# Performance work log

Measured on AMD Instinct MI355X. Metric: run time of the kernel, lower is better.

The kernel has to match this reference:

```python
import jax, jax.numpy as jnp
import numpy as np

B, A, NC, DIR, LMAX, MAXZ, NORB = 8, 64, 128, 4, 2, 10, 14
NF = NC * DIR * (2 * LMAX + 1)   # 2560
O2 = NORB * NORB                 # 196
AO = A * NORB                    # 896
LOG2 = float(np.log(2.0))

def ssp(v):  # spk shifted softplus
    return jax.nn.softplus(v) - LOG2

def setup_inputs():
    key = jax.random.key(0)
    ks = jax.random.split(key, 12)
    Z = jax.random.randint(ks[0], (B, A), 1, MAXZ)
    idx = np.arange(A)
    nbh_np = np.stack([np.delete(idx, i) for i in range(A)], 0)  # [A, A-1]: all atoms except self
    nbh = jnp.asarray(np.broadcast_to(nbh_np[None], (B, A, A - 1)).copy(), dtype=jnp.int32)
    x = jax.random.normal(ks[1], (B, A, NC), jnp.float32)
    Vijkl = jax.random.normal(ks[2], (B, A, A - 1, NF), jnp.float32) * 0.1
    sc = 1.0 / np.sqrt(NF)
    W_off = jax.random.normal(ks[3], (NF, O2), jnp.float32) * sc
    b_off = jnp.zeros((O2,), jnp.float32)
    W_on = jax.random.normal(ks[4], (NF, O2), jnp.float32) * sc
    b_on = jnp.zeros((O2,), jnp.float32)
    W_ovoff = jax.random.normal(ks[5], (NF, O2), jnp.float32) * sc
    b_ovoff = jnp.zeros((O2,), jnp.float32)
    ov_emb = jax.random.normal(ks[6], (MAXZ, O2), jnp.float32) * 0.1  # trainable overlap onsite embedding
    orb_energies = jax.random.normal(ks[7], (MAXZ, NORB), jnp.float32)  # h0 energies
    s0_energies = jnp.ones((MAXZ, NORB), jnp.float32)                   # s0 init = ones
    W1 = jax.random.normal(ks[8], (NC, NC // 2), jnp.float32) / np.sqrt(NC)
    b1 = jnp.zeros((NC // 2,), jnp.float32)
    W2 = jax.random.normal(ks[9], (NC // 2, 1), jnp.float32) / np.sqrt(NC // 2)
    b2 = jnp.zeros((1,), jnp.float32)
    return {"Z": Z, "nbh": nbh, "x": x, "Vijkl": Vijkl,
            "W_off": W_off, "b_off": b_off, "W_on": W_on, "b_on": b_on,
            "W_ovoff": W_ovoff, "b_ovoff": b_ovoff, "ov_emb": ov_emb,
            "orb_energies": orb_energies, "s0_energies": s0_energies,
            "W1": W1, "b1": b1, "W2": W2, "b2": b2}

def reference(Z, nbh, x, Vijkl, W_off, b_off, W_on, b_on, W_ovoff, b_ovoff,
              ov_emb, orb_energies, s0_energies, W1, b1, W2, b2):
    # permutation that reorders neighbor slots (plus appended zero/self slot) into atom order
    ar = jnp.broadcast_to(jnp.arange(A, dtype=nbh.dtype)[None, :, None], (B, A, 1))
    sort_idx = jnp.argsort(jnp.concatenate([nbh, ar], axis=2), axis=2)  # [B,A,A]
    eyeA = jnp.eye(A, dtype=Vijkl.dtype)
    eyeAO = jnp.eye(AO, dtype=Vijkl.dtype)

    def assemble(off, on):
        # off: [B,A,A-1,O2] pair blocks; on: [B,A,O2] onsite blocks
        offz = jnp.concatenate([off, jnp.zeros((B, A, 1, O2), off.dtype)], axis=2)  # zero self block at slot A-1
        offg = jnp.take_along_axis(offz, sort_idx[..., None], axis=2)               # [B,A,A,O2]
        M = offg + eyeA[None, :, :, None] * on[:, :, None, :]
        M = M.reshape(B, A, A, NORB, NORB).transpose(0, 1, 3, 2, 4).reshape(B, AO, AO)
        return 0.5 * (M + M.transpose(0, 2, 1))

    # Hamiltonian: offsite Dense + onsite Dense mean-aggregated over pairs
    H_off = Vijkl @ W_off + b_off                       # [B,A,A-1,O2]
    H_on = jnp.mean(Vijkl @ W_on + b_on, axis=2)        # [B,A,O2]
    H = assemble(H_off, H_on)
    # h0 single-atom diagonal (orb mask is all-active -> full diagonal)
    H = H + eyeAO[None] * orb_energies[Z].reshape(B, 1, AO)

    # Overlap: offsite Dense + onsite embedding lookup
    S_off = Vijkl @ W_ovoff + b_ovoff
    S_on = ov_emb[Z]                                    # [B,A,O2]
    S = assemble(S_off, S_on)
    S = S + eyeAO[None] * s0_energies[Z].reshape(B, 1, AO)

    # energy head: Dense->ssp->Dense->ScaleShift(0,1), sum over atoms
    Ei = ssp(x @ W1 + b1) @ W2 + b2                     # [B,A,1]
    E = jnp.sum(Ei, axis=1)                             # [B,1]
    return H, S, E
```

## Files before the change

### kernel.cpp

```cpp
#include <hip/hip_runtime.h>

#define B_      8
#define A_      64
#define NPAIR   63
#define NC_     128
#define NF_     2560
#define O2_     196
#define NORB_   14
#define AO_     896
#define NCOLS   588
#define CSTRIDE 640
#define KSTEPS  80
#define BM      128
#define BN      640
#define BSTEP_BYTES 40960

typedef short bf16x8 __attribute__((ext_vector_type(8)));
typedef float f32x4  __attribute__((ext_vector_type(4)));

__device__ __forceinline__ unsigned f2bf(float f) {
    unsigned u = __builtin_bit_cast(unsigned, f);
    return (u + 0x7fffu + ((u >> 16) & 1u)) >> 16;
}

__global__ void prep_w(const float* __restrict__ W_off, const float* __restrict__ W_ovoff,
                       const float* __restrict__ W_on, unsigned short* __restrict__ Bws) {
    __shared__ float wt[32 * BN];
    const int ks = blockIdx.x, t = threadIdx.x;
    for (int e = t; e < 32 * BN; e += 256) {
        int kl = e / BN, c = e - kl * BN;
        int kg = ks * 32 + kl;
        float v = 0.f;
        if (c < O2_)          v = W_off  [(size_t)kg * O2_ + c];
        else if (c < 2 * O2_) v = W_ovoff[(size_t)kg * O2_ + (c - O2_)];
        else if (c < 3 * O2_) v = W_on   [(size_t)kg * O2_ + (c - 2 * O2_)];
        wt[kl * BN + c] = v;
    }
    __syncthreads();
    unsigned short* out = Bws + (size_t)ks * (BN * 32);
    for (int e = t; e < BN * 4; e += 256) {
        int n = e >> 2, sg = e & 3;
        uint4 w;
        w.x = f2bf(wt[(sg * 8 + 0) * BN + n]) | (f2bf(wt[(sg * 8 + 1) * BN + n]) << 16);
        w.y = f2bf(wt[(sg * 8 + 2) * BN + n]) | (f2bf(wt[(sg * 8 + 3) * BN + n]) << 16);
        w.z = f2bf(wt[(sg * 8 + 4) * BN + n]) | (f2bf(wt[(sg * 8 + 5) * BN + n]) << 16);
        w.w = f2bf(wt[(sg * 8 + 6) * BN + n]) | (f2bf(wt[(sg * 8 + 7) * BN + n]) << 16);
        *(uint4*)(out + (size_t)n * 32 + sg * 8) = w;
    }
}

__global__ __launch_bounds__(512, 2)
void gemm_off(const float* __restrict__ V, const unsigned short* __restrict__ Bws,
              const float* __restrict__ b_off, const float* __restrict__ b_ovoff,
              const float* __restrict__ b_on, float* __restrict__ HSoff) {
    __shared__ alignas(16) unsigned short Alds[2][BM * 32];

    const int tid  = threadIdx.x;
    const int mt   = blockIdx.x;
    const int lane = tid & 63;
    const int wv   = tid >> 6;
    const int wm   = wv >> 2, wn = wv & 3;

    const int arow = tid >> 2, aseg = tid & 3;
    const float* aptr = V + (size_t)(mt * BM + arow) * NF_ + aseg * 8;

    const char* bp = (const char*)Bws + (size_t)(wn * 160 + (lane & 15)) * 64 + (lane >> 4) * 16;
#define BFRAG(t_, nf_) (*(const bf16x8*)(bp + (size_t)(t_) * BSTEP_BYTES + (nf_) * 1024))

    f32x4 acc[4][10];
#pragma unroll
    for (int mf = 0; mf < 4; ++mf)
#pragma unroll
        for (int nf = 0; nf < 10; ++nf)
            acc[mf][nf] = (f32x4){0.f, 0.f, 0.f, 0.f};

    float4 pv0, pv1;
    auto loadA = [&](int ks) {
        const float* s = aptr + ks * 32;
        pv0 = ((const float4*)s)[0];
        pv1 = ((const float4*)s)[1];
    };
    auto writeA = [&](int bf) {
        uint4 w;
        w.x = f2bf(pv0.x) | (f2bf(pv0.y) << 16);
        w.y = f2bf(pv0.z) | (f2bf(pv0.w) << 16);
        w.z = f2bf(pv1.x) | (f2bf(pv1.y) << 16);
        w.w = f2bf(pv1.z) | (f2bf(pv1.w) << 16);
        unsigned byte = ((unsigned)(arow * 64 + aseg * 16)) ^ ((unsigned)(arow & 7) << 4);
        *(uint4*)((char*)&Alds[bf][0] + byte) = w;
    };

    const int ar = wm * 64 + (lane & 15);
    const unsigned kb = (unsigned)(lane >> 4) * 16;

#define ARD(mf_) (*(const bf16x8*)((const char*)Ab + ((((unsigned)((ar + (mf_) * 16) * 64) + kb)) ^ ((unsigned)(ar & 7) << 4))))

#define MFMA4(bv_, nf_) {                                                                  \
    acc[0][nf_] = __builtin_amdgcn_mfma_f32_16x16x32_bf16(af0, bv_, acc[0][nf_], 0, 0, 0); \
    acc[1][nf_] = __builtin_amdgcn_mfma_f32_16x16x32_bf16(af1, bv_, acc[1][nf_], 0, 0, 0); \
    acc[2][nf_] = __builtin_amdgcn_mfma_f32_16x16x32_bf16(af2, bv_, acc[2][nf_], 0, 0, 0); \
    acc[3][nf_] = __builtin_amdgcn_mfma_f32_16x16x32_bf16(af3, bv_, acc[3][nf_], 0, 0, 0); }

    bf16x8 bq0, bq1, bq2, bq3, bq4;

    loadA(0);
    writeA(0);
    bq0 = BFRAG(0, 0); bq1 = BFRAG(0, 1); bq2 = BFRAG(0, 2); bq3 = BFRAG(0, 3); bq4 = BFRAG(0, 4);
    loadA(1);
    asm volatile("s_waitcnt lgkmcnt(0)" ::: "memory");
    __builtin_amdgcn_s_barrier();
    __builtin_amdgcn_sched_barrier(0);

    int cur = 0;
    for (int t = 0; t < KSTEPS; ++t) {
        const unsigned short* Ab = &Alds[cur][0];
        bf16x8 af0 = ARD(0), af1 = ARD(1), af2 = ARD(2), af3 = ARD(3);

        MFMA4(bq0, 0); bq0 = BFRAG(t, 5);
        MFMA4(bq1, 1); bq1 = BFRAG(t, 6);
        MFMA4(bq2, 2); bq2 = BFRAG(t, 7);
        MFMA4(bq3, 3); bq3 = BFRAG(t, 8);
        MFMA4(bq4, 4); bq4 = BFRAG(t, 9);
        MFMA4(bq0, 5); bq0 = BFRAG(t + 1, 0);
        MFMA4(bq1, 6); bq1 = BFRAG(t + 1, 1);
        MFMA4(bq2, 7); bq2 = BFRAG(t + 1, 2);
        MFMA4(bq3, 8); bq3 = BFRAG(t + 1, 3);
        MFMA4(bq4, 9); bq4 = BFRAG(t + 1, 4);

        if (t < KSTEPS - 1) {
            writeA(cur ^ 1);
            int ks2 = t + 2 < KSTEPS ? t + 2 : KSTEPS - 1;
            loadA(ks2);
            asm volatile("s_waitcnt lgkmcnt(0)" ::: "memory");
            __builtin_amdgcn_s_barrier();
            __builtin_amdgcn_sched_barrier(0);
        }
        cur ^= 1;
    }

    const int c16 = lane & 15, rg = lane >> 4;
#pragma unroll
    for (int nf = 0; nf < 10; ++nf) {
        int C = wn * 160 + nf * 16 + c16;
        if (C >= NCOLS) continue;
        float bias = (C < O2_) ? b_off[C] : (C < 2 * O2_) ? b_ovoff[C - O2_] : b_on[C - 2 * O2_];
#pragma unroll
        for (int mf = 0; mf < 4; ++mf) {
            int R = mt * BM + wm * 64 + mf * 16 + rg * 4;
            float* o = HSoff + (size_t)R * CSTRIDE + C;
            o[0]           = acc[mf][nf][0] + bias;
            o[CSTRIDE]     = acc[mf][nf][1] + bias;
            o[2 * CSTRIDE] = acc[mf][nf][2] + bias;
            o[3 * CSTRIDE] = acc[mf][nf][3] + bias;
        }
    }
#undef BFRAG
#undef ARD
#undef MFMA4
}

__global__ void hon_reduce(const float* __restrict__ HSoff, float* __restrict__ Hon) {
    const int g = blockIdx.x;
    const int t = threadIdx.x;
    if (t >= O2_) return;
    const float* p0 = HSoff + (size_t)g * NPAIR * CSTRIDE + 2 * O2_ + t;
    const float* p1 = p0 + (size_t)21 * CSTRIDE;
    const float* p2 = p0 + (size_t)42 * CSTRIDE;
    float a0 = 0.f, a1 = 0.f, a2 = 0.f;
#pragma unroll 3
    for (int j = 0; j < 21; ++j) {
        a0 += p0[0]; a1 += p1[0]; a2 += p2[0];
        p0 += CSTRIDE; p1 += CSTRIDE; p2 += CSTRIDE;
    }
    Hon[(size_t)g * O2_ + t] = (a0 + a1 + a2) * (1.f / (float)NPAIR);
}

__global__ __launch_bounds__(256)
void assemble_k(const float* __restrict__ HSoff, const float* __restrict__ Hon,
                const int* __restrict__ Z, const float* __restrict__ ov_emb,
                const float* __restrict__ orbE, const float* __restrict__ s0E,
                float* __restrict__ H, float* __restrict__ S) {
    __shared__ float Ai[NPAIR * 197];
    __shared__ float Bj[2][16 * 200];
    __shared__ float Dg[O2_];
    __shared__ float Dd[NORB_];

    const int bid = blockIdx.x;
    const int h = bid & 1, i = (bid >> 1) & 63, b = bid >> 7;
    const int t = threadIdx.x;
    const int g = b * A_ + i;
    const int z = Z[g];
    float* out = (h ? S : H) + (size_t)b * AO_ * AO_;

    const float* abase = HSoff + (size_t)g * NPAIR * CSTRIDE + h * O2_;
    for (int u = t; u < NPAIR * O2_; u += 256) {
        int jj = u / O2_, e = u - jj * O2_;
        Ai[jj * 197 + e] = abase[(size_t)jj * CSTRIDE + e];
    }
    if (t < O2_)   Dg[t] = h ? ov_emb[(size_t)z * O2_ + t]   : Hon[(size_t)g * O2_ + t];
    if (t < NORB_) Dd[t] = h ? s0E[(size_t)z * NORB_ + t]    : orbE[(size_t)z * NORB_ + t];

    auto stageB = [&](int buf, int jc) {
        for (int u = t; u < 16 * O2_; u += 256) {
            int jl = u / O2_, e = u - jl * O2_;
            int j = jc * 16 + jl;
            if (j != i) {
                int idx = (i < j) ? i : i - 1;
                Bj[buf][jl * 200 + e] =
                    HSoff[((size_t)(b * A_ + j) * NPAIR + idx) * CSTRIDE + h * O2_ + e];
            }
        }
    };
    stageB(0, 0);
    __syncthreads();

    const int tj = t / NORB_, tq = t - tj * NORB_;
    for (int jc = 0; jc < 4; ++jc) {
        if (jc < 3) stageB((jc + 1) & 1, jc + 1);
        if (t < 224) {
            const int j = jc * 16 + tj;
            const int cur = jc & 1;
#pragma unroll
            for (int p = 0; p < NORB_; ++p) {
                float v;
                if (j == i) {
                    v = 0.5f * (Dg[p * NORB_ + tq] + Dg[tq * NORB_ + p]);
                    if (p == tq) v += Dd[p];
                } else {
                    int jj = (j < i) ? j : j - 1;
                    v = 0.5f * (Ai[jj * 197 + p * NORB_ + tq] + Bj[cur][tj * 200 + tq * NORB_ + p]);
                }
                out[(size_t)(i * NORB_ + p) * AO_ + jc * 224 + t] = v;
            }
        }
        __syncthreads();
    }
}

__global__ void energy_k(const float* __restrict__ x, const float* __restrict__ W1,
                         const float* __restrict__ b1, const float* __restrict__ W2,
                         const float* __restrict__ b2, float* __restrict__ E) {
    __shared__ float partial[8];
    const int b = blockIdx.x;
    const int lane = threadIdx.x & 63;
    const int w = threadIdx.x >> 6;
    float esum = 0.f;
    for (int aa = 0; aa < 8; ++aa) {
        const int a = w * 8 + aa;
        const float* xr = x + (size_t)(b * A_ + a) * NC_;
        float hj = b1[lane];
        for (int k = 0; k < NC_; ++k) hj = fmaf(xr[k], W1[k * 64 + lane], hj);
        float sp = fmaxf(hj, 0.f) + log1pf(expf(-fabsf(hj))) - 0.69314718055994531f;
        float v = sp * W2[lane];
        for (int off = 32; off; off >>= 1) v += __shfl_down(v, off);
        if (lane == 0) esum += v + b2[0];
    }
    if (lane == 0) partial[w] = esum;
    __syncthreads();
    if (threadIdx.x == 0) {
        float e = 0.f;
        for (int k = 0; k < 8; ++k) e += partial[k];
        E[b] = e;
    }
}

extern "C" void kernel_launch(void* const* d_in, const int* in_sizes, int n_in,
                              void* d_out, int out_size, void* d_ws, size_t ws_size,
                              hipStream_t stream) {
    const int*   Z       = (const int*)  d_in[0];
    const float* x       = (const float*)d_in[2];
    const float* V       = (const float*)d_in[3];
    const float* W_off   = (const float*)d_in[4];
    const float* b_off   = (const float*)d_in[5];
    const float* W_on    = (const float*)d_in[6];
    const float* b_on    = (const float*)d_in[7];
    const float* W_ovoff = (const float*)d_in[8];
    const float* b_ovoff = (const float*)d_in[9];
    const float* ov_emb  = (const float*)d_in[10];
    const float* orbE    = (const float*)d_in[11];
    const float* s0E     = (const float*)d_in[12];
    const float* W1      = (const float*)d_in[13];
    const float* b1      = (const float*)d_in[14];
    const float* W2      = (const float*)d_in[15];
    const float* b2      = (const float*)d_in[16];

    float* H = (float*)d_out;
    float* S = H + (size_t)B_ * AO_ * AO_;
    float* E = S + (size_t)B_ * AO_ * AO_;

    char* ws = (char*)d_ws;
    unsigned short* Bws = (unsigned short*)ws;
    float* HSoff = (float*)(ws + (size_t)4  * 1024 * 1024);
    float* Hon   = (float*)(ws + (size_t)88 * 1024 * 1024);

    prep_w    <<<KSTEPS, 256, 0, stream>>>(W_off, W_ovoff, W_on, Bws);
    gemm_off  <<<252,    512, 0, stream>>>(V, Bws, b_off, b_ovoff, b_on, HSoff);
    hon_reduce<<<512,    256, 0, stream>>>(HSoff, Hon);
    assemble_k<<<1024,   256, 0, stream>>>(HSoff, Hon, Z, ov_emb, orbE, s0E, H, S);
    energy_k  <<<8,      512, 0, stream>>>(x, W1, b1, W2, b2, E);
}
```

Measured before the change: 307.5 us.

## Halve GEMM M-tile to 64 rows and fuse energy head into weight-prep kernel

The GEMM row tile drops from 128 to 64, so the grid doubles to 504 blocks and each wave holds half as many accumulators. Launch bounds rise to 4 blocks per SM, and the A-tile staging and swizzle indexing are reworked to match. The aim is to fill more of the CUs, since 252 blocks leave many idle, at the cost of reloading each B fragment for fewer rows. The energy head is merged into the weight-prep kernel as extra blocks to save one launch.

Measured after the change: 361.5 us. 17.6% more time.

```diff
diff --git a/kernel.cpp b/kernel.cpp
--- a/kernel.cpp
+++ b/kernel.cpp
@@ -11,7 +11,7 @@
 #define NCOLS   588
 #define CSTRIDE 640
 #define KSTEPS  80
-#define BM      128
+#define BM      64
 #define BN      640
 #define BSTEP_BYTES 40960
 
@@ -23,33 +23,63 @@
     return (u + 0x7fffu + ((u >> 16) & 1u)) >> 16;
 }
 
-__global__ void prep_w(const float* __restrict__ W_off, const float* __restrict__ W_ovoff,
-                       const float* __restrict__ W_on, unsigned short* __restrict__ Bws) {
-    __shared__ float wt[32 * BN];
-    const int ks = blockIdx.x, t = threadIdx.x;
-    for (int e = t; e < 32 * BN; e += 256) {
-        int kl = e / BN, c = e - kl * BN;
-        int kg = ks * 32 + kl;
-        float v = 0.f;
-        if (c < O2_)          v = W_off  [(size_t)kg * O2_ + c];
-        else if (c < 2 * O2_) v = W_ovoff[(size_t)kg * O2_ + (c - O2_)];
-        else if (c < 3 * O2_) v = W_on   [(size_t)kg * O2_ + (c - 2 * O2_)];
-        wt[kl * BN + c] = v;
-    }
-    __syncthreads();
-    unsigned short* out = Bws + (size_t)ks * (BN * 32);
-    for (int e = t; e < BN * 4; e += 256) {
-        int n = e >> 2, sg = e & 3;
-        uint4 w;
-        w.x = f2bf(wt[(sg * 8 + 0) * BN + n]) | (f2bf(wt[(sg * 8 + 1) * BN + n]) << 16);
-        w.y = f2bf(wt[(sg * 8 + 2) * BN + n]) | (f2bf(wt[(sg * 8 + 3) * BN + n]) << 16);
-        w.z = f2bf(wt[(sg * 8 + 4) * BN + n]) | (f2bf(wt[(sg * 8 + 5) * BN + n]) << 16);
-        w.w = f2bf(wt[(sg * 8 + 6) * BN + n]) | (f2bf(wt[(sg * 8 + 7) * BN + n]) << 16);
-        *(uint4*)(out + (size_t)n * 32 + sg * 8) = w;
-    }
-}
-
-__global__ __launch_bounds__(512, 2)
+__global__ __launch_bounds__(512)
+void prep_energy(const float* __restrict__ W_off, const float* __restrict__ W_ovoff,
+                 const float* __restrict__ W_on, unsigned short* __restrict__ Bws,
+                 const float* __restrict__ x, const float* __restrict__ W1,
+                 const float* __restrict__ b1, const float* __restrict__ W2,
+                 const float* __restrict__ b2, float* __restrict__ E) {
+    const int t = threadIdx.x;
+    if (blockIdx.x < KSTEPS) {
+        __shared__ float wt[32 * BN];
+        const int ks = blockIdx.x;
+        for (int e = t; e < 32 * BN; e += 512) {
+            int kl = e / BN, c = e - kl * BN;
+            int kg = ks * 32 + kl;
+            float v = 0.f;
+            if (c < O2_)          v = W_off  [(size_t)kg * O2_ + c];
+            else if (c < 2 * O2_) v = W_ovoff[(size_t)kg * O2_ + (c - O2_)];
+            else if (c < 3 * O2_) v = W_on   [(size_t)kg * O2_ + (c - 2 * O2_)];
+            wt[kl * BN + c] = v;
+        }
+        __syncthreads();
+        unsigned short* out = Bws + (size_t)ks * (BN * 32);
+        for (int e = t; e < BN * 4; e += 512) {
+            int n = e >> 2, sg = e & 3;
+            uint4 w;
+            w.x = f2bf(wt[(sg * 8 + 0) * BN + n]) | (f2bf(wt[(sg * 8 + 1) * BN + n]) << 16);
+            w.y = f2bf(wt[(sg * 8 + 2) * BN + n]) | (f2bf(wt[(sg * 8 + 3) * BN + n]) << 16);
+            w.z = f2bf(wt[(sg * 8 + 4) * BN + n]) | (f2bf(wt[(sg * 8 + 5) * BN + n]) << 16);
+            w.w = f2bf(wt[(sg * 8 + 6) * BN + n]) | (f2bf(wt[(sg * 8 + 7) * BN + n]) << 16);
+            *(uint4*)(out + (size_t)n * 32 + sg * 8) = w;
+        }
+    } else {
+        __shared__ float partial[8];
+        const int b = blockIdx.x - KSTEPS;
+        const int lane = t & 63;
+        const int w = t >> 6;
+        float esum = 0.f;
+        for (int aa = 0; aa < 8; ++aa) {
+            const int a = w * 8 + aa;
+            const float* xr = x + (size_t)(b * A_ + a) * NC_;
+            float hj = b1[lane];
+            for (int k = 0; k < NC_; ++k) hj = fmaf(xr[k], W1[k * 64 + lane], hj);
+            float sp = fmaxf(hj, 0.f) + log1pf(expf(-fabsf(hj))) - 0.69314718055994531f;
+            float v = sp * W2[lane];
+            for (int off = 32; off; off >>= 1) v += __shfl_down(v, off);
+            if (lane == 0) esum += v + b2[0];
+        }
+        if (lane == 0) partial[w] = esum;
+        __syncthreads();
+        if (t == 0) {
+            float e = 0.f;
+            for (int k = 0; k < 8; ++k) e += partial[k];
+            E[b] = e;
+        }
+    }
+}
+
+__global__ __launch_bounds__(512, 4)
 void gemm_off(const float* __restrict__ V, const unsigned short* __restrict__ Bws,
               const float* __restrict__ b_off, const float* __restrict__ b_ovoff,
               const float* __restrict__ b_on, float* __restrict__ HSoff) {
@@ -61,45 +91,39 @@
     const int wv   = tid >> 6;
     const int wm   = wv >> 2, wn = wv & 3;
 
-    const int arow = tid >> 2, aseg = tid & 3;
-    const float* aptr = V + (size_t)(mt * BM + arow) * NF_ + aseg * 8;
+    const int arow = tid >> 3, aseg = tid & 7;
+    const float* aptr = V + (size_t)(mt * BM + arow) * NF_ + aseg * 4;
 
     const char* bp = (const char*)Bws + (size_t)(wn * 160 + (lane & 15)) * 64 + (lane >> 4) * 16;
 #define BFRAG(t_, nf_) (*(const bf16x8*)(bp + (size_t)(t_) * BSTEP_BYTES + (nf_) * 1024))
 
-    f32x4 acc[4][10];
-#pragma unroll
-    for (int mf = 0; mf < 4; ++mf)
+    f32x4 acc[2][10];
+#pragma unroll
+    for (int mf = 0; mf < 2; ++mf)
 #pragma unroll
         for (int nf = 0; nf < 10; ++nf)
             acc[mf][nf] = (f32x4){0.f, 0.f, 0.f, 0.f};
 
-    float4 pv0, pv1;
+    float4 pv;
     auto loadA = [&](int ks) {
-        const float* s = aptr + ks * 32;
-        pv0 = ((const float4*)s)[0];
-        pv1 = ((const float4*)s)[1];
+        pv = *(const float4*)(aptr + ks * 32);
     };
     auto writeA = [&](int bf) {
-        uint4 w;
-        w.x = f2bf(pv0.x) | (f2bf(pv0.y) << 16);
-        w.y = f2bf(pv0.z) | (f2bf(pv0.w) << 16);
-        w.z = f2bf(pv1.x) | (f2bf(pv1.y) << 16);
-        w.w = f2bf(pv1.z) | (f2bf(pv1.w) << 16);
-        unsigned byte = ((unsigned)(arow * 64 + aseg * 16)) ^ ((unsigned)(arow & 7) << 4);
-        *(uint4*)((char*)&Alds[bf][0] + byte) = w;
+        uint2 w;
+        w.x = f2bf(pv.x) | (f2bf(pv.y) << 16);
+        w.y = f2bf(pv.z) | (f2bf(pv.w) << 16);
+        unsigned byte = ((unsigned)(arow * 64 + aseg * 8)) ^ ((unsigned)(arow & 7) << 4);
+        *(uint2*)((char*)&Alds[bf][0] + byte) = w;
     };
 
-    const int ar = wm * 64 + (lane & 15);
+    const int ar = wm * 32 + (lane & 15);
     const unsigned kb = (unsigned)(lane >> 4) * 16;
 
-#define ARD(mf_) (*(const bf16x8*)((const char*)Ab + ((((unsigned)((ar + (mf_) * 16) * 64) + kb)) ^ ((unsigned)(ar & 7) << 4))))
-
-#define MFMA4(bv_, nf_) {                                                                  \
+#define ARD(mf_) (*(const bf16x8*)((const char*)Ab + ((((unsigned)((ar + (mf_) * 16) * 64) + kb)) ^ ((unsigned)((ar + (mf_) * 16) & 7) << 4))))
+
+#define MFMA2(bv_, nf_) {                                                                  \
     acc[0][nf_] = __builtin_amdgcn_mfma_f32_16x16x32_bf16(af0, bv_, acc[0][nf_], 0, 0, 0); \
-    acc[1][nf_] = __builtin_amdgcn_mfma_f32_16x16x32_bf16(af1, bv_, acc[1][nf_], 0, 0, 0); \
-    acc[2][nf_] = __builtin_amdgcn_mfma_f32_16x16x32_bf16(af2, bv_, acc[2][nf_], 0, 0, 0); \
-    acc[3][nf_] = __builtin_amdgcn_mfma_f32_16x16x32_bf16(af3, bv_, acc[3][nf_], 0, 0, 0); }
+    acc[1][nf_] = __builtin_amdgcn_mfma_f32_16x16x32_bf16(af1, bv_, acc[1][nf_], 0, 0, 0); }
 
     bf16x8 bq0, bq1, bq2, bq3, bq4;
 
@@ -114,18 +138,18 @@
     int cur = 0;
     for (int t = 0; t < KSTEPS; ++t) {
         const unsigned short* Ab = &Alds[cur][0];
-        bf16x8 af0 = ARD(0), af1 = ARD(1), af2 = ARD(2), af3 = ARD(3);
-
-        MFMA4(bq0, 0); bq0 = BFRAG(t, 5);
-        MFMA4(bq1, 1); bq1 = BFRAG(t, 6);
-        MFMA4(bq2, 2); bq2 = BFRAG(t, 7);
-        MFMA4(bq3, 3); bq3 = BFRAG(t, 8);
-        MFMA4(bq4, 4); bq4 = BFRAG(t, 9);
-        MFMA4(bq0, 5); bq0 = BFRAG(t + 1, 0);
-        MFMA4(bq1, 6); bq1 = BFRAG(t + 1, 1);
-        MFMA4(bq2, 7); bq2 = BFRAG(t + 1, 2);
-        MFMA4(bq3, 8); bq3 = BFRAG(t + 1, 3);
-        MFMA4(bq4, 9); bq4 = BFRAG(t + 1, 4);
+        bf16x8 af0 = ARD(0), af1 = ARD(1);
+
+        MFMA2(bq0, 0); bq0 = BFRAG(t, 5);
+        MFMA2(bq1, 1); bq1 = BFRAG(t, 6);
+        MFMA2(bq2, 2); bq2 = BFRAG(t, 7);
+        MFMA2(bq3, 3); bq3 = BFRAG(t, 8);
+        MFMA2(bq4, 4); bq4 = BFRAG(t, 9);
+        MFMA2(bq0, 5); bq0 = BFRAG(t + 1, 0);
+        MFMA2(bq1, 6); bq1 = BFRAG(t + 1, 1);
+        MFMA2(bq2, 7); bq2 = BFRAG(t + 1, 2);
+        MFMA2(bq3, 8); bq3 = BFRAG(t + 1, 3);
+        MFMA2(bq4, 9); bq4 = BFRAG(t + 1, 4);
 
         if (t < KSTEPS - 1) {
             writeA(cur ^ 1);
@@ -145,8 +169,8 @@
         if (C >= NCOLS) continue;
         float bias = (C < O2_) ? b_off[C] : (C < 2 * O2_) ? b_ovoff[C - O2_] : b_on[C - 2 * O2_];
 #pragma unroll
-        for (int mf = 0; mf < 4; ++mf) {
-            int R = mt * BM + wm * 64 + mf * 16 + rg * 4;
+        for (int mf = 0; mf < 2; ++mf) {
+            int R = mt * BM + wm * 32 + mf * 16 + rg * 4;
             float* o = HSoff + (size_t)R * CSTRIDE + C;
             o[0]           = acc[mf][nf][0] + bias;
             o[CSTRIDE]     = acc[mf][nf][1] + bias;
@@ -156,7 +180,7 @@
     }
 #undef BFRAG
 #undef ARD
-#undef MFMA4
+#undef MFMA2
 }
 
 __global__ void hon_reduce(const float* __restrict__ HSoff, float* __restrict__ Hon) {
@@ -234,33 +258,6 @@
             }
         }
         __syncthreads();
-    }
-}
-
-__global__ void energy_k(const float* __restrict__ x, const float* __restrict__ W1,
-                         const float* __restrict__ b1, const float* __restrict__ W2,
-                         const float* __restrict__ b2, float* __restrict__ E) {
-    __shared__ float partial[8];
-    const int b = blockIdx.x;
-    const int lane = threadIdx.x & 63;
-    const int w = threadIdx.x >> 6;
-    float esum = 0.f;
-    for (int aa = 0; aa < 8; ++aa) {
-        const int a = w * 8 + aa;
-        const float* xr = x + (size_t)(b * A_ + a) * NC_;
-        float hj = b1[lane];
-        for (int k = 0; k < NC_; ++k) hj = fmaf(xr[k], W1[k * 64 + lane], hj);
-        float sp = fmaxf(hj, 0.f) + log1pf(expf(-fabsf(hj))) - 0.69314718055994531f;
-        float v = sp * W2[lane];
-        for (int off = 32; off; off >>= 1) v += __shfl_down(v, off);
-        if (lane == 0) esum += v + b2[0];
-    }
-    if (lane == 0) partial[w] = esum;
-    __syncthreads();
-    if (threadIdx.x == 0) {
-        float e = 0.f;
-        for (int k = 0; k < 8; ++k) e += partial[k];
-        E[b] = e;
     }
 }
 
@@ -293,9 +290,9 @@
     float* HSoff = (float*)(ws + (size_t)4  * 1024 * 1024);
     float* Hon   = (float*)(ws + (size_t)88 * 1024 * 1024);
 
-    prep_w    <<<KSTEPS, 256, 0, stream>>>(W_off, W_ovoff, W_on, Bws);
-    gemm_off  <<<252,    512, 0, stream>>>(V, Bws, b_off, b_ovoff, b_on, HSoff);
-    hon_reduce<<<512,    256, 0, stream>>>(HSoff, Hon);
-    assemble_k<<<1024,   256, 0, stream>>>(HSoff, Hon, Z, ov_emb, orbE, s0E, H, S);
-    energy_k  <<<8,      512, 0, stream>>>(x, W1, b1, W2, b2, E);
-}
+    prep_energy<<<KSTEPS + B_, 512, 0, stream>>>(W_off, W_ovoff, W_on, Bws,
+                                                 x, W1, b1, W2, b2, E);
+    gemm_off   <<<504,  512, 0, stream>>>(V, Bws, b_off, b_ovoff, b_on, HSoff);
+    hon_reduce <<<512,  256, 0, stream>>>(HSoff, Hon);
+    assemble_k <<<1024, 256, 0, stream>>>(HSoff, Hon, Z, ov_emb, orbE, s0E, H, S);
+}
```
